# Optimization experiments

Hardware: AMD Instinct MI355X
Metric: run time of the kernel (lower is better)

Reference implementation:

```python
import jax, jax.numpy as jnp
import numpy as np

N_NODES = 100000


def _deg_norm(idx, n):
    # inverse-sqrt degree, zero-degree nodes -> 0 (DGL norm='both' convention)
    deg = jax.ops.segment_sum(jnp.ones(idx.shape, jnp.float32), idx, num_segments=n)
    return jnp.where(deg > 0, jax.lax.rsqrt(jnp.maximum(deg, 1.0)), 0.0)


def graph_conv(x, src, dst, W, b, n):
    # symmetric normalization: D_out^{-1/2} on src, D_in^{-1/2} on dst
    norm_src = _deg_norm(src, n)  # [N]
    norm_dst = _deg_norm(dst, n)  # [N]
    h = (x * norm_src[:, None]) @ W          # apply weight first (in >= out)
    msg = h[src]                              # gather [E, out]
    agg = jax.ops.segment_sum(msg, dst, num_segments=n)  # scatter-add [N, out]
    return agg * norm_dst[:, None] + b


def setup_inputs() -> dict:
    key = jax.random.key(0)
    ks = jax.random.split(key, 6)
    x = jax.random.normal(ks[0], (N_NODES, 128), dtype=jnp.float32)
    edge_index = jax.random.randint(ks[1], (2, 1600000), 0, N_NODES, dtype=jnp.int64)
    W1 = jax.random.normal(ks[2], (128, 64), dtype=jnp.float32) * (1.0 / np.sqrt(128))
    b1 = jnp.zeros((64,), jnp.float32)
    W2 = jax.random.normal(ks[3], (64, 32), dtype=jnp.float32) * (1.0 / np.sqrt(64))
    b2 = jnp.zeros((32,), jnp.float32)
    Wl = jax.random.normal(ks[4], (32, 1), dtype=jnp.float32) * (1.0 / np.sqrt(32))
    bl = jnp.zeros((1,), jnp.float32)
    return {"x": x, "edge_index": edge_index, "W1": W1, "b1": b1,
            "W2": W2, "b2": b2, "Wl": Wl, "bl": bl}


def reference(x, edge_index, W1, b1, W2, b2, Wl, bl):
    src, dst = edge_index[0], edge_index[1]
    n = x.shape[0]
    h = graph_conv(x, src, dst, W1, b1, n)
    h = jax.nn.relu(h)
    # dropout(p=0.5) is identity at inference
    h = graph_conv(h, src, dst, W2, b2, n)
    return h @ Wl + bl  # [N, 1]
```

## Files before the change

kernel.cpp:

```cpp
#include <hip/hip_runtime.h>
#include <hip/hip_fp16.h>


#define WAVE 64
#define NRANGE 8
#define NQUAD 2
#define CB 1024
#define CHK 32
#define RB (CB / CHK)

typedef _Float16 f16x8 __attribute__((ext_vector_type(8)));
typedef float f32x4 __attribute__((ext_vector_type(4)));

__global__ __launch_bounds__(256) void k_cnt(const int* __restrict__ dst,
                                             unsigned* __restrict__ cnt,
                                             int E, int B, int chunkEb,
                                             const float* __restrict__ W1,
                                             const float* __restrict__ W2,
                                             const float* __restrict__ b2,
                                             const float* __restrict__ Wl,
                                             const float* __restrict__ bl,
                                             _Float16* __restrict__ wt,
                                             float* __restrict__ w2l,
                                             float* __restrict__ c0) {
    if (blockIdx.x == CB) {
        int t = threadIdx.x;
        for (int i = 0; i < 32; ++i) {
            int e = i * 256 + t;
            int k = e >> 6, n = e & 63;
            wt[n * 128 + k] = (_Float16)W1[e];
        }
        if (t < 64) {
            float acc = 0.f;
#pragma unroll
            for (int j = 0; j < 32; ++j) acc += W2[t * 32 + j] * Wl[j];
            w2l[t] = acc;
        }
        if (t == 0) {
            float s = 0.f;
#pragma unroll
            for (int j = 0; j < 32; ++j) s += b2[j] * Wl[j];
            *c0 = s + bl[0];
        }
        return;
    }
    __shared__ unsigned lc[NRANGE];
    if (threadIdx.x < NRANGE) lc[threadIdx.x] = 0u;
    __syncthreads();
    const int c = blockIdx.x;
    const int beg = c * chunkEb, end = min(beg + chunkEb, E);
    unsigned pc[NRANGE] = {};
    for (int i = beg + (int)threadIdx.x; i < end; i += 256) {
        int r = dst[i] / B;
#pragma unroll
        for (int rr = 0; rr < NRANGE; ++rr) pc[rr] += (r == rr);
    }
#pragma unroll
    for (int rr = 0; rr < NRANGE; ++rr) {
        unsigned v = pc[rr];
#pragma unroll
        for (int off = 32; off; off >>= 1) v += __shfl_xor((int)v, off);
        if ((threadIdx.x & 63) == 0 && v) atomicAdd(&lc[rr], v);
    }
    __syncthreads();
    if (threadIdx.x < NRANGE) cnt[threadIdx.x * CB + c] = lc[threadIdx.x];
}

__global__ __launch_bounds__(256) void k_scancnt2(const unsigned* __restrict__ cnt,
                                                  unsigned* __restrict__ segBase,
                                                  unsigned* __restrict__ rangeCur,
                                                  int SLOT) {
    __shared__ unsigned s[256];
    const int t = threadIdx.x;
    const int PER = (NRANGE * CB) / 256;
    unsigned loc[PER];
    unsigned sum = 0;
#pragma unroll
    for (int j = 0; j < PER; ++j) { loc[j] = sum; sum += cnt[t * PER + j]; }
    s[t] = sum;
    __syncthreads();
    for (int off = 1; off < 256; off <<= 1) {
        unsigned a = (t >= off) ? s[t - off] : 0u;
        __syncthreads();
        s[t] += a;
        __syncthreads();
    }
    unsigned base = s[t] - sum;
#pragma unroll
    for (int j = 0; j < PER; ++j) segBase[t * PER + j] = base + loc[j];
    if (t == 255) segBase[NRANGE * CB] = s[255];
    if (t < NRANGE) rangeCur[t] = (unsigned)(t * SLOT);
}

__global__ __launch_bounds__(256) void k_hist(const int* __restrict__ srcArr,
                                              const int* __restrict__ dstArr,
                                              unsigned* __restrict__ partial_s,
                                              unsigned* __restrict__ partial_d,
                                              int E, int B, int chunkE) {
    extern __shared__ unsigned hist[];
    const int q = blockIdx.x & (NQUAD - 1);
    const int c = blockIdx.x >> 1;
    const int lo = q * 4 * B;
    const int* nodes = blockIdx.y ? dstArr : srcArr;
    unsigned* partial = blockIdx.y ? partial_d : partial_s;

    for (int b = threadIdx.x; b < B; b += 256) hist[b] = 0u;
    __syncthreads();

    const int beg = c * chunkE, end = min(beg + chunkE, E);
    const int n4 = (end - beg) >> 2;
    const int4* p = (const int4*)(nodes + beg);
    for (int j = threadIdx.x; j < n4; j += 256) {
        int4 v = p[j];
#pragma unroll
        for (int k = 0; k < 4; ++k) {
            int a = (&v.x)[k] - lo;
            if ((unsigned)a < (unsigned)(4 * B)) {
                int h2 = (a >= 2 * B);
                int r2 = a - (h2 ? 2 * B : 0);
                int h1 = (r2 >= B);
                int bin = r2 - (h1 ? B : 0);
                atomicAdd(&hist[bin], 1u << (((h2 << 1) | h1) << 3));
            }
        }
    }
    for (int j = beg + (n4 << 2) + threadIdx.x; j < end; j += 256) {
        int a = nodes[j] - lo;
        if ((unsigned)a < (unsigned)(4 * B)) {
            int h2 = (a >= 2 * B);
            int r2 = a - (h2 ? 2 * B : 0);
            int h1 = (r2 >= B);
            int bin = r2 - (h1 ? B : 0);
            atomicAdd(&hist[bin], 1u << (((h2 << 1) | h1) << 3));
        }
    }
    __syncthreads();
    unsigned* outp = partial + (size_t)(q * CHK + c) * B;
    for (int b = threadIdx.x; b < B; b += 256) outp[b] = hist[b];
}

__global__ __launch_bounds__(256) void k_bucket(const int* __restrict__ src,
                                                const int* __restrict__ dst,
                                                const unsigned* __restrict__ segBase,
                                                uint2* __restrict__ ebuf,
                                                int E, int B, int chunkEb) {
    __shared__ unsigned lcnt[NRANGE];
    const int c = blockIdx.x;
    const int lane = threadIdx.x & 63;
    if (threadIdx.x < NRANGE) lcnt[threadIdx.x] = 0u;
    __syncthreads();

    unsigned sb[NRANGE];
#pragma unroll
    for (int r = 0; r < NRANGE; ++r) sb[r] = segBase[r * CB + c];

    const int beg = c * chunkEb, end = min(beg + chunkEb, E);
    for (int i = beg + (int)threadIdx.x; i < end; i += 256) {
        int d = dst[i];
        int s = src[i];
        int r = d / B;
#pragma unroll
        for (int rr = 0; rr < NRANGE; ++rr) {
            unsigned long long m = __ballot(r == rr);
            if (m) {
                int leader = __ffsll((long long)m) - 1;
                unsigned base = 0;
                if (lane == leader) base = atomicAdd(&lcnt[rr], (unsigned)__popcll(m));
                base = (unsigned)__shfl((int)base, leader);
                if (r == rr) {
                    unsigned before = (unsigned)__popcll(m & ((1ull << lane) - 1ull));
                    ebuf[sb[rr] + base + before] = make_uint2((unsigned)s, (unsigned)d);
                }
            }
        }
    }
}

__global__ __launch_bounds__(256) void k_reduce_norm(const unsigned* __restrict__ partial_s,
                                                     unsigned* __restrict__ partial_d,
                                                     float* __restrict__ norm_s,
                                                     float* __restrict__ norm_d,
                                                     unsigned* __restrict__ deg_d,
                                                     unsigned* __restrict__ offsets,
                                                     unsigned* __restrict__ rangeCur,
                                                     int N, int B, int Bpad) {
    int t = blockIdx.x * 256 + threadIdx.x;
    int lane = threadIdx.x & 63;
    int q = t / Bpad, b = t - q * Bpad;
    bool valid = (q < NQUAD) && (b < B);
    unsigned ds = 0, run = 0;
    if (valid) {
        size_t base = (size_t)(q * CHK) * B + b;
        for (int c = 0; c < CHK; ++c) ds += partial_s[base + (size_t)c * B];
        unsigned acc = 0;
        for (int c = 0; c < CHK; ++c) {
            size_t ix = base + (size_t)c * B;
            unsigned v = partial_d[ix];
            partial_d[ix] = acc;
            acc += v;
        }
        run = acc;
    }
#pragma unroll
    for (int j = 0; j < 4; ++j) {
        unsigned d1 = valid ? ((run >> (8 * j)) & 0xffu) : 0u;
        unsigned p = d1;
#pragma unroll
        for (int off = 1; off < 64; off <<= 1) {
            unsigned o = (unsigned)__shfl_up((int)p, off);
            if (lane >= off) p += o;
        }
        unsigned tot = (unsigned)__shfl((int)p, 63);
        int r = q * 4 + j;
        unsigned wbase = 0;
        if (lane == 63 && tot) wbase = atomicAdd(&rangeCur[r], tot);
        wbase = (unsigned)__shfl((int)wbase, 63);
        if (valid) {
            int n = q * 4 * B + j * B + b;
            if (n < N) {
                unsigned d0 = (ds >> (8 * j)) & 0xffu;
                deg_d[n] = d1;
                norm_s[n] = d0 ? rsqrtf((float)d0) : 0.0f;
                norm_d[n] = d1 ? rsqrtf((float)d1) : 0.0f;
                offsets[n] = wbase + (p - d1);
            }
        }
    }
}

__global__ __launch_bounds__(256) void k_fill2(const uint2* __restrict__ ebuf,
                                               const unsigned* __restrict__ segBase,
                                               const unsigned* __restrict__ offsets,
                                               const unsigned* __restrict__ rel,
                                               unsigned* __restrict__ csr,
                                               int N, int B) {
    extern __shared__ unsigned curs[];
    const int r = blockIdx.x & (NRANGE - 1);
    const int ch = blockIdx.x >> 3;
    const int lo = r * B;
    const int bins = min(B, N - lo);
    const int sh = (r & 3) << 3;
    const unsigned* relp = rel + (size_t)((r >> 2) * CHK + ch) * B;
    for (int b = threadIdx.x; b < bins; b += 256)
        curs[b] = offsets[lo + b] + ((relp[b] >> sh) & 0xffu);
    __syncthreads();

    const unsigned s0 = segBase[r * CB + ch * RB];
    const unsigned s1 = segBase[r * CB + ch * RB + RB];
    for (unsigned i = s0 + threadIdx.x; i < s1; i += 256) {
        uint2 e = ebuf[i];
        int a = (int)e.y - lo;
        if ((unsigned)a < (unsigned)bins)
            csr[atomicAdd(&curs[a], 1u)] = e.x;
    }
}

__global__ __launch_bounds__(256) void k_gemm1(const float* __restrict__ x,
                                               const _Float16* __restrict__ wt,
                                               const float* __restrict__ norm_s,
                                               __half* __restrict__ h1h, int N) {
    __shared__ __align__(16) _Float16 xs[64 * 128];
    const int tid = threadIdx.x, lane = tid & 63, wv = tid >> 6;
    const int r0 = blockIdx.x * 64;

    f16x8 bf[4][4];
#pragma unroll
    for (int kt = 0; kt < 4; ++kt)
#pragma unroll
        for (int nt = 0; nt < 4; ++nt)
            bf[kt][nt] = *(const f16x8*)&wt[(nt * 16 + (lane & 15)) * 128 +
                                            kt * 32 + (lane >> 4) * 8];

#pragma unroll
    for (int it = 0; it < 8; ++it) {
        int e = it * 256 + tid;
        int r = e >> 5, c = e & 31;
        int row = r0 + r;
        float4 v = (row < N) ? ((const float4*)x)[(size_t)row * 32 + c]
                             : make_float4(0.f, 0.f, 0.f, 0.f);
        __half2 lo2 = __floats2half2_rn(v.x, v.y);
        __half2 hi2 = __floats2half2_rn(v.z, v.w);
        uint2 pk;
        pk.x = *(unsigned*)&lo2;
        pk.y = *(unsigned*)&hi2;
        int byte = r * 256 + c * 8;
        byte ^= (r & 7) << 4;
        *(uint2*)((char*)xs + byte) = pk;
    }
    __syncthreads();

    f32x4 acc[4] = {};
    const int rloc = wv * 16 + (lane & 15);
#pragma unroll
    for (int kt = 0; kt < 4; ++kt) {
        int byte = rloc * 256 + (kt * 32 + (lane >> 4) * 8) * 2;
        byte ^= (rloc & 7) << 4;
        f16x8 af = *(const f16x8*)((char*)xs + byte);
#pragma unroll
        for (int nt = 0; nt < 4; ++nt)
            acc[nt] = __builtin_amdgcn_mfma_f32_16x16x32_f16(af, bf[kt][nt], acc[nt], 0, 0, 0);
    }

#pragma unroll
    for (int j = 0; j < 4; ++j) {
        int row = r0 + wv * 16 + (lane >> 4) * 4 + j;
        if (row < N) {
            float ns = norm_s[row];
#pragma unroll
            for (int nt = 0; nt < 4; ++nt)
                h1h[(size_t)row * 64 + nt * 16 + (lane & 15)] =
                    __float2half(acc[nt][j] * ns);
        }
    }
}

__global__ __launch_bounds__(256) void k_agg_rdot(const unsigned* __restrict__ offsets,
                                                  const unsigned* __restrict__ deg_d,
                                                  const unsigned* __restrict__ csr,
                                                  const __half* __restrict__ h1h,
                                                  const float* __restrict__ norm_s,
                                                  const float* __restrict__ norm_d,
                                                  const float* __restrict__ b1,
                                                  const float* __restrict__ w2l,
                                                  float* __restrict__ s_node, int N) {
    const int lane = threadIdx.x & 63;
    const int slot = lane >> 4;
    const int p = lane & 15;
    const int v = (blockIdx.x * 256 + threadIdx.x) >> 6;
    if (v >= N) return;
    const unsigned beg = offsets[v];
    const unsigned end = beg + deg_d[v];

    float a0 = 0.f, a1 = 0.f, a2 = 0.f, a3 = 0.f;
#define GATHER(sreg) { \
        uint2 u = *(const uint2*)&h1h[(size_t)(sreg) * 64 + 4 * p]; \
        float2 f0 = __half22float2(*(__half2*)&u.x); \
        float2 f1 = __half22float2(*(__half2*)&u.y); \
        a0 += f0.x; a1 += f0.y; a2 += f1.x; a3 += f1.y; }

    for (unsigned base = beg; base < end; base += WAVE) {
        const int n = (int)min((unsigned)WAVE, end - base);
        int sv = (lane < n) ? (int)csr[base + lane] : 0;
        int i = 0;
        for (; i + 32 <= n; i += 32) {
            int s0 = __shfl(sv, i + 0 + slot);
            int s1 = __shfl(sv, i + 4 + slot);
            int s2 = __shfl(sv, i + 8 + slot);
            int s3 = __shfl(sv, i + 12 + slot);
            int s4 = __shfl(sv, i + 16 + slot);
            int s5 = __shfl(sv, i + 20 + slot);
            int s6 = __shfl(sv, i + 24 + slot);
            int s7 = __shfl(sv, i + 28 + slot);
            GATHER(s0); GATHER(s1); GATHER(s2); GATHER(s3);
            GATHER(s4); GATHER(s5); GATHER(s6); GATHER(s7);
        }
        for (; i + 16 <= n; i += 16) {
            int s0 = __shfl(sv, i + 0 + slot);
            int s1 = __shfl(sv, i + 4 + slot);
            int s2 = __shfl(sv, i + 8 + slot);
            int s3 = __shfl(sv, i + 12 + slot);
            GATHER(s0); GATHER(s1); GATHER(s2); GATHER(s3);
        }
        for (; i < n; i += 4) {
            int e = i + slot;
            int s = __shfl(sv, min(e, n - 1));
            if (e < n) GATHER(s);
        }
    }
#undef GATHER
    a0 += __shfl_xor(a0, 16); a0 += __shfl_xor(a0, 32);
    a1 += __shfl_xor(a1, 16); a1 += __shfl_xor(a1, 32);
    a2 += __shfl_xor(a2, 16); a2 += __shfl_xor(a2, 32);
    a3 += __shfl_xor(a3, 16); a3 += __shfl_xor(a3, 32);

    float nd = norm_d[v];
    float4 bq = *(const float4*)&b1[4 * p];
    float4 wq = *(const float4*)&w2l[4 * p];
    float t = fmaxf(fmaf(a0, nd, bq.x), 0.f) * wq.x
            + fmaxf(fmaf(a1, nd, bq.y), 0.f) * wq.y
            + fmaxf(fmaf(a2, nd, bq.z), 0.f) * wq.z
            + fmaxf(fmaf(a3, nd, bq.w), 0.f) * wq.w;
#pragma unroll
    for (int off = 8; off; off >>= 1) t += __shfl_xor(t, off);
    if (lane == 0) s_node[v] = t * norm_s[v];
}

__global__ __launch_bounds__(256) void k_out(const unsigned* __restrict__ offsets,
                                             const unsigned* __restrict__ deg_d,
                                             const unsigned* __restrict__ csr,
                                             const float* __restrict__ s_node,
                                             const float* __restrict__ norm_d,
                                             const float* __restrict__ c0,
                                             float* __restrict__ out, int N) {
    int v = blockIdx.x * 256 + threadIdx.x;
    if (v >= N) return;
    unsigned beg = offsets[v], end = beg + deg_d[v];
    float sum = 0.f;
    unsigned j = beg;
    for (; j + 4 <= end; j += 4) {
        float a = s_node[csr[j + 0]], b = s_node[csr[j + 1]];
        float c = s_node[csr[j + 2]], d = s_node[csr[j + 3]];
        sum += (a + b) + (c + d);
    }
    for (; j < end; ++j) sum += s_node[csr[j]];
    out[v] = fmaf(sum, norm_d[v], *c0);
}

extern "C" void kernel_launch(void* const* d_in, const int* in_sizes, int n_in,
                              void* d_out, int out_size, void* d_ws, size_t ws_size,
                              hipStream_t stream) {
    const float* x  = (const float*)d_in[0];
    const int*   ei = (const int*)d_in[1];
    const float* W1 = (const float*)d_in[2];
    const float* b1 = (const float*)d_in[3];
    const float* W2 = (const float*)d_in[4];
    const float* b2 = (const float*)d_in[5];
    const float* Wl = (const float*)d_in[6];
    const float* bl = (const float*)d_in[7];

    const int N = in_sizes[0] / 128;
    const int E = in_sizes[1] / 2;
    const int* src = ei;
    const int* dst = ei + E;
    const int NB = (N + 255) / 256;
    const int B = (N + NRANGE - 1) / NRANGE;
    const int Bpad = ((B + 63) / 64) * 64;
    const int SLOT = E / NRANGE + 16384;
    const int chunkEb = (E + CB - 1) / CB;
    const int chunkE = chunkEb * RB;

    char* w = (char*)d_ws;
    auto alloc = [&](size_t bytes) -> void* {
        void* r = (void*)w;
        w += (bytes + 255) & ~(size_t)255;
        return r;
    };
    float*    norm_s    = (float*)alloc((size_t)N * 4);
    float*    norm_d    = (float*)alloc((size_t)N * 4);
    unsigned* deg_d     = (unsigned*)alloc((size_t)N * 4);
    unsigned* offsets   = (unsigned*)alloc((size_t)N * 4);
    __half*   h1h       = (__half*)alloc((size_t)N * 64 * 2);
    unsigned* csr       = (unsigned*)alloc((size_t)NRANGE * SLOT * 4);
    float*    s_node    = (float*)alloc((size_t)N * 4);
    float*    w2l       = (float*)alloc(64 * 4);
    float*    c0        = (float*)alloc(4);
    _Float16* wt        = (_Float16*)alloc(64 * 128 * 2);
    uint2*    ebuf      = (uint2*)alloc((size_t)E * 8);
    unsigned* cnt       = (unsigned*)alloc((size_t)(NRANGE * CB + 1) * 4);
    unsigned* segBase   = (unsigned*)alloc((size_t)(NRANGE * CB + 1) * 4);
    unsigned* rangeCur  = (unsigned*)alloc(NRANGE * 4);
    unsigned* partial_s = (unsigned*)alloc((size_t)NQUAD * CHK * B * 4);
    unsigned* partial_d = (unsigned*)alloc((size_t)NQUAD * CHK * B * 4);

    float* out = (float*)d_out;
    const size_t ldsB = (size_t)B * 4;

    k_cnt<<<CB + 1, 256, 0, stream>>>(dst, cnt, E, B, chunkEb,
                                      W1, W2, b2, Wl, bl, wt, w2l, c0);
    k_scancnt2<<<1, 256, 0, stream>>>(cnt, segBase, rangeCur, SLOT);
    k_hist<<<dim3(NQUAD * CHK, 2), 256, ldsB, stream>>>(src, dst, partial_s,
                                                        partial_d, E, B, chunkE);
    k_bucket<<<CB, 256, 0, stream>>>(src, dst, segBase, ebuf, E, B, chunkEb);

    k_reduce_norm<<<(NQUAD * Bpad + 255) / 256, 256, 0, stream>>>(
        partial_s, partial_d, norm_s, norm_d, deg_d, offsets, rangeCur,
        N, B, Bpad);

    k_gemm1<<<(N + 63) / 64, 256, 0, stream>>>(x, wt, norm_s, h1h, N);

    k_fill2<<<NRANGE * CHK, 256, ldsB, stream>>>(ebuf, segBase, offsets,
                                                 partial_d, csr, N, B);

    k_agg_rdot<<<(N + 3) / 4, 256, 0, stream>>>(offsets, deg_d, csr, h1h,
                                                norm_s, norm_d, b1, w2l,
                                                s_node, N);
    k_out<<<NB, 256, 0, stream>>>(offsets, deg_d, csr, s_node, norm_d, c0, out, N);
}
```

Before: 188.5 us.

## Pack bucketed edges into 32-bit words, split degree reduction, parallelize final gather

Bucketed edges are now stored as one 32-bit word (local bin in the high bits, source index in the low 17 bits) instead of a uint2 pair. This halves edge-buffer write and read traffic in the bucket and fill kernels. The degree-reduction kernel now uses separate thread groups for the source-degree sum and the destination-degree prefix scan, doubling its parallelism. The final output gather uses four lanes per node with a shuffle reduction. The packing assumes fewer than 2^17 nodes and a bin below 2^15.

Result: faster. 184.3 us (median of 2 runs) (-2.2%).

```diff
diff --git a/kernel.cpp b/kernel.cpp
--- a/kernel.cpp
+++ b/kernel.cpp
@@ -142,7 +142,7 @@
 __global__ __launch_bounds__(256) void k_bucket(const int* __restrict__ src,
                                                 const int* __restrict__ dst,
                                                 const unsigned* __restrict__ segBase,
-                                                uint2* __restrict__ ebuf,
+                                                unsigned* __restrict__ ebuf,
                                                 int E, int B, int chunkEb) {
     __shared__ unsigned lcnt[NRANGE];
     const int c = blockIdx.x;
@@ -159,6 +159,7 @@
         int d = dst[i];
         int s = src[i];
         int r = d / B;
+        unsigned pk = ((unsigned)(d - r * B) << 17) | (unsigned)s;
 #pragma unroll
         for (int rr = 0; rr < NRANGE; ++rr) {
             unsigned long long m = __ballot(r == rr);
@@ -169,7 +170,7 @@
                 base = (unsigned)__shfl((int)base, leader);
                 if (r == rr) {
                     unsigned before = (unsigned)__popcll(m & ((1ull << lane) - 1ull));
-                    ebuf[sb[rr] + base + before] = make_uint2((unsigned)s, (unsigned)d);
+                    ebuf[sb[rr] + base + before] = pk;
                 }
             }
         }
@@ -186,49 +187,64 @@
                                                      int N, int B, int Bpad) {
     int t = blockIdx.x * 256 + threadIdx.x;
     int lane = threadIdx.x & 63;
-    int q = t / Bpad, b = t - q * Bpad;
-    bool valid = (q < NQUAD) && (b < B);
-    unsigned ds = 0, run = 0;
-    if (valid) {
+    const int half = NQUAD * Bpad;
+    if (t < half) {
+        int q = t / Bpad, b = t - q * Bpad;
+        bool valid = (b < B);
+        unsigned run = 0;
+        if (valid) {
+            size_t base = (size_t)(q * CHK) * B + b;
+            unsigned acc = 0;
+            for (int c = 0; c < CHK; ++c) {
+                size_t ix = base + (size_t)c * B;
+                unsigned v = partial_d[ix];
+                partial_d[ix] = acc;
+                acc += v;
+            }
+            run = acc;
+        }
+#pragma unroll
+        for (int j = 0; j < 4; ++j) {
+            unsigned d1 = valid ? ((run >> (8 * j)) & 0xffu) : 0u;
+            unsigned p = d1;
+#pragma unroll
+            for (int off = 1; off < 64; off <<= 1) {
+                unsigned o = (unsigned)__shfl_up((int)p, off);
+                if (lane >= off) p += o;
+            }
+            unsigned tot = (unsigned)__shfl((int)p, 63);
+            int r = q * 4 + j;
+            unsigned wbase = 0;
+            if (lane == 63 && tot) wbase = atomicAdd(&rangeCur[r], tot);
+            wbase = (unsigned)__shfl((int)wbase, 63);
+            if (valid) {
+                int n = q * 4 * B + j * B + b;
+                if (n < N) {
+                    deg_d[n] = d1;
+                    norm_d[n] = d1 ? rsqrtf((float)d1) : 0.0f;
+                    offsets[n] = wbase + (p - d1);
+                }
+            }
+        }
+    } else {
+        t -= half;
+        int q = t / Bpad, b = t - q * Bpad;
+        if (q >= NQUAD || b >= B) return;
         size_t base = (size_t)(q * CHK) * B + b;
+        unsigned ds = 0;
         for (int c = 0; c < CHK; ++c) ds += partial_s[base + (size_t)c * B];
-        unsigned acc = 0;
-        for (int c = 0; c < CHK; ++c) {
-            size_t ix = base + (size_t)c * B;
-            unsigned v = partial_d[ix];
-            partial_d[ix] = acc;
-            acc += v;
-        }
-        run = acc;
-    }
-#pragma unroll
-    for (int j = 0; j < 4; ++j) {
-        unsigned d1 = valid ? ((run >> (8 * j)) & 0xffu) : 0u;
-        unsigned p = d1;
-#pragma unroll
-        for (int off = 1; off < 64; off <<= 1) {
-            unsigned o = (unsigned)__shfl_up((int)p, off);
-            if (lane >= off) p += o;
-        }
-        unsigned tot = (unsigned)__shfl((int)p, 63);
-        int r = q * 4 + j;
-        unsigned wbase = 0;
-        if (lane == 63 && tot) wbase = atomicAdd(&rangeCur[r], tot);
-        wbase = (unsigned)__shfl((int)wbase, 63);
-        if (valid) {
+#pragma unroll
+        for (int j = 0; j < 4; ++j) {
             int n = q * 4 * B + j * B + b;
             if (n < N) {
                 unsigned d0 = (ds >> (8 * j)) & 0xffu;
-                deg_d[n] = d1;
                 norm_s[n] = d0 ? rsqrtf((float)d0) : 0.0f;
-                norm_d[n] = d1 ? rsqrtf((float)d1) : 0.0f;
-                offsets[n] = wbase + (p - d1);
-            }
-        }
-    }
-}
-
-__global__ __launch_bounds__(256) void k_fill2(const uint2* __restrict__ ebuf,
+            }
+        }
+    }
+}
+
+__global__ __launch_bounds__(256) void k_fill2(const unsigned* __restrict__ ebuf,
                                                const unsigned* __restrict__ segBase,
                                                const unsigned* __restrict__ offsets,
                                                const unsigned* __restrict__ rel,
@@ -248,10 +264,10 @@
     const unsigned s0 = segBase[r * CB + ch * RB];
     const unsigned s1 = segBase[r * CB + ch * RB + RB];
     for (unsigned i = s0 + threadIdx.x; i < s1; i += 256) {
-        uint2 e = ebuf[i];
-        int a = (int)e.y - lo;
-        if ((unsigned)a < (unsigned)bins)
-            csr[atomicAdd(&curs[a], 1u)] = e.x;
+        unsigned e = ebuf[i];
+        unsigned bin = e >> 17;
+        if (bin < (unsigned)bins)
+            csr[atomicAdd(&curs[bin], 1u)] = e & 0x1ffffu;
     }
 }
 
@@ -392,18 +408,16 @@
                                              const float* __restrict__ norm_d,
                                              const float* __restrict__ c0,
                                              float* __restrict__ out, int N) {
-    int v = blockIdx.x * 256 + threadIdx.x;
+    int t = blockIdx.x * 256 + threadIdx.x;
+    int v = t >> 2, slot = t & 3;
     if (v >= N) return;
     unsigned beg = offsets[v], end = beg + deg_d[v];
     float sum = 0.f;
-    unsigned j = beg;
-    for (; j + 4 <= end; j += 4) {
-        float a = s_node[csr[j + 0]], b = s_node[csr[j + 1]];
-        float c = s_node[csr[j + 2]], d = s_node[csr[j + 3]];
-        sum += (a + b) + (c + d);
-    }
-    for (; j < end; ++j) sum += s_node[csr[j]];
-    out[v] = fmaf(sum, norm_d[v], *c0);
+    for (unsigned j = beg + slot; j < end; j += 4)
+        sum += s_node[csr[j]];
+    sum += __shfl_xor(sum, 1);
+    sum += __shfl_xor(sum, 2);
+    if (slot == 0) out[v] = fmaf(sum, norm_d[v], *c0);
 }
 
 extern "C" void kernel_launch(void* const* d_in, const int* in_sizes, int n_in,
@@ -422,7 +436,6 @@
     const int E = in_sizes[1] / 2;
     const int* src = ei;
     const int* dst = ei + E;
-    const int NB = (N + 255) / 256;
     const int B = (N + NRANGE - 1) / NRANGE;
     const int Bpad = ((B + 63) / 64) * 64;
     const int SLOT = E / NRANGE + 16384;
@@ -445,7 +458,7 @@
     float*    w2l       = (float*)alloc(64 * 4);
     float*    c0        = (float*)alloc(4);
     _Float16* wt        = (_Float16*)alloc(64 * 128 * 2);
-    uint2*    ebuf      = (uint2*)alloc((size_t)E * 8);
+    unsigned* ebuf      = (unsigned*)alloc((size_t)E * 4);
     unsigned* cnt       = (unsigned*)alloc((size_t)(NRANGE * CB + 1) * 4);
     unsigned* segBase   = (unsigned*)alloc((size_t)(NRANGE * CB + 1) * 4);
     unsigned* rangeCur  = (unsigned*)alloc(NRANGE * 4);
@@ -462,7 +475,7 @@
                                                         partial_d, E, B, chunkE);
     k_bucket<<<CB, 256, 0, stream>>>(src, dst, segBase, ebuf, E, B, chunkEb);
 
-    k_reduce_norm<<<(NQUAD * Bpad + 255) / 256, 256, 0, stream>>>(
+    k_reduce_norm<<<(2 * NQUAD * Bpad + 255) / 256, 256, 0, stream>>>(
         partial_s, partial_d, norm_s, norm_d, deg_d, offsets, rangeCur,
         N, B, Bpad);
 
@@ -474,5 +487,6 @@
     k_agg_rdot<<<(N + 3) / 4, 256, 0, stream>>>(offsets, deg_d, csr, h1h,
                                                 norm_s, norm_d, b1, w2l,
                                                 s_node, N);
-    k_out<<<NB, 256, 0, stream>>>(offsets, deg_d, csr, s_node, norm_d, c0, out, N);
-}
+    k_out<<<(4 * N + 255) / 256, 256, 0, stream>>>(offsets, deg_d, csr, s_node,
+                                                   norm_d, c0, out, N);
+}
```
